# Performance work log

Measured on AMD Instinct MI355X. Metric: run time of the kernel, lower is better.

The kernel has to match this reference:

```python
import jax, jax.numpy as jnp
import numpy as np

EMB = 1024
HEAD = 64
B = 4
S = 4096


def setup_inputs() -> dict:
    key = jax.random.key(0)
    ks = jax.random.split(key, 7)
    std = 1.0 / np.sqrt(EMB)
    return {
        "x": jax.random.normal(ks[0], (B, S, EMB), dtype=jnp.float32),
        "Wq": jax.random.uniform(ks[1], (EMB, HEAD), jnp.float32, -std, std),
        "bq": jax.random.uniform(ks[2], (HEAD,), jnp.float32, -std, std),
        "Wk": jax.random.uniform(ks[3], (EMB, HEAD), jnp.float32, -std, std),
        "bk": jax.random.uniform(ks[4], (HEAD,), jnp.float32, -std, std),
        "Wv": jax.random.uniform(ks[5], (EMB, HEAD), jnp.float32, -std, std),
        "bv": jax.random.uniform(ks[6], (HEAD,), jnp.float32, -std, std),
    }


def reference(x, Wq, bq, Wk, bk, Wv, bv):
    # Q, K, V: [B, S, HEAD]
    Q = x @ Wq + bq
    K = x @ Wk + bk
    V = x @ Wv + bv
    scale = 1.0 / jnp.sqrt(jnp.asarray(HEAD, dtype=Q.dtype))
    # scores: [B, S, S]
    scores = jnp.einsum("bqd,bkd->bqk", Q, K) * scale
    seq = x.shape[1]
    # original mask = tril(randn) sliced; masked_fill where mask==0 => causal
    causal = jnp.tril(jnp.ones((seq, seq), dtype=bool))
    scores = jnp.where(causal, scores, -jnp.inf)
    attn = jax.nn.softmax(scores, axis=-1)
    return jnp.einsum("bqk,bkd->bqd", attn, V)
```

## Files before the change

### kernel.cpp

```cpp
#include <hip/hip_runtime.h>
#include <stdint.h>

#define S_LEN 4096
#define EMB   1024
#define HEAD  64

typedef short bf16x8 __attribute__((ext_vector_type(8)));
typedef float f32x4  __attribute__((ext_vector_type(4)));
typedef float f32x16 __attribute__((ext_vector_type(16)));

#define QSCALE 0.18033688011112042f

__device__ __forceinline__ unsigned short f2bf(float f) {
    union { float f; uint32_t u; } v; v.f = f;
    uint32_t r = v.u + 0x7fffu + ((v.u >> 16) & 1u);
    return (unsigned short)(r >> 16);
}

__device__ __forceinline__ int cvtpk_bf16(float lo, float hi_) {
    int r;
    asm("v_cvt_pk_bf16_f32 %0, %1, %2" : "=v"(r) : "v"(lo), "v"(hi_));
    return r;
}

__device__ __forceinline__ void gload_lds16(const void* g, void* l) {
    __builtin_amdgcn_global_load_lds(
        (const __attribute__((address_space(1))) void*)g,
        (__attribute__((address_space(3))) void*)l, 16, 0, 0);
}


__global__ void wprep_kernel(const float* __restrict__ Wq,
                             const float* __restrict__ Wk,
                             const float* __restrict__ Wv,
                             unsigned short* __restrict__ wt) {
    __shared__ float t[64][65];
    const int tid = threadIdx.x;
    const int m   = blockIdx.x >> 4;
    const int kcb = blockIdx.x & 15;
    const int k0  = kcb << 6;
    const float* W = (m == 0) ? Wq : (m == 1) ? Wk : Wv;
    for (int i = 0; i < 4; ++i) {
        const int k  = (tid >> 4) + i * 16;
        const int n4 = (tid & 15) << 2;
        float4 v = *(const float4*)&W[(k0 + k) * 64 + n4];
        t[k][n4 + 0] = v.x; t[k][n4 + 1] = v.y;
        t[k][n4 + 2] = v.z; t[k][n4 + 3] = v.w;
    }
    __syncthreads();
    const int n = tid >> 2, kq = (tid & 3) << 4;
    __align__(16) unsigned short u[16];
    for (int i = 0; i < 16; ++i) u[i] = f2bf(t[kq + i][n]);
    const int nimg = m * 64 + n;
    const int base = kcb * 12288 + nimg * 64;
    const int c0   = (kq >> 3) ^ (n & 7);
    const int c1   = ((kq >> 3) + 1) ^ (n & 7);
    *(int4*)&wt[base + c0 * 8] = *(int4*)&u[0];
    *(int4*)&wt[base + c1 * 8] = *(int4*)&u[8];
}

__global__ __launch_bounds__(512, 2) void qkv_kernel(
    const float* __restrict__ x, const unsigned short* __restrict__ wt,
    const float* __restrict__ bq, const float* __restrict__ bk,
    const float* __restrict__ bv,
    unsigned short* __restrict__ Qp, unsigned short* __restrict__ Kp,
    unsigned short* __restrict__ Vt) {

    __shared__ __align__(16) unsigned short xs[2][32 * 72];
    __shared__ __align__(16) unsigned short ws[2][12288];

    const int tid  = threadIdx.x;
    const int lane = tid & 63;
    const int w    = tid >> 6;
    const int wm   = w & 1;
    const int wn   = w >> 1;
    const int quad = lane >> 4;
    const int lid  = lane & 15;
    const int row0 = blockIdx.x * 32;

    f32x4 acc[3];
    for (int nf = 0; nf < 3; ++nf) acc[nf] = (f32x4){0.f, 0.f, 0.f, 0.f};

#define STAGE(BUF, KC)                                                         \
    do {                                                                       \
        {           \
            int rr = tid >> 4, c4 = (tid & 15) << 2;                           \
            float4 v = *(const float4*)&x[(row0 + rr) * EMB + (KC) * 64 + c4]; \
            ushort4 u;                                                         \
            u.x = f2bf(v.x); u.y = f2bf(v.y); u.z = f2bf(v.z); u.w = f2bf(v.w);\
            *(ushort4*)&xs[BUF][rr * 72 + c4] = u;                             \
        }                                                                      \
        {          \
            const unsigned short* gs = &wt[(KC) * 12288 + w * 1536 + lane * 8];\
            gload_lds16(gs,        &ws[BUF][w * 1536]);                        \
            gload_lds16(gs +  512, &ws[BUF][w * 1536 +  512]);                 \
            gload_lds16(gs + 1024, &ws[BUF][w * 1536 + 1024]);                 \
        }                                                                      \
    } while (0)

    STAGE(0, 0);
    __syncthreads();

    for (int kc = 0; kc < 16; ++kc) {
        const int cur = kc & 1;
        if (kc + 1 < 16) STAGE(cur ^ 1, kc + 1);
        for (int kk = 0; kk < 2; ++kk) {
            bf16x8 a = *(const bf16x8*)&xs[cur][(wm * 16 + lid) * 72 + kk * 32 + quad * 8];
            const int swz = ((((kk << 2) | quad) ^ (lid & 7)) << 3);
            for (int nf = 0; nf < 3; ++nf) {
                const int n = wn * 48 + nf * 16 + lid;
                bf16x8 bfr = *(const bf16x8*)&ws[cur][n * 64 + swz];
                acc[nf] = __builtin_amdgcn_mfma_f32_16x16x32_bf16(a, bfr, acc[nf], 0, 0, 0);
            }
        }
        __syncthreads();
    }
#undef STAGE

    for (int nf = 0; nf < 3; ++nf) {
        const int col = wn * 48 + nf * 16 + lid;
        const int mid = col >> 6;
        const int lc  = col & 63;
        const float bias = (mid == 0) ? bq[lc] : (mid == 1) ? bk[lc] : bv[lc];
        const int rb = row0 + wm * 16 + quad * 4;
        f32x4 v = acc[nf];
        if (mid < 2) {
            const int base = ((rb >> 5) << 11) + ((lc >> 3) << 8)
                           + ((rb & 31) << 3) + (lc & 7);
            unsigned short* P = (mid == 0) ? Qp : Kp;
            const float sc = (mid == 0) ? QSCALE : 1.0f;
            for (int j = 0; j < 4; ++j)
                P[base + j * 8] = f2bf((v[j] + bias) * sc);
        } else {
            const int bb = rb >> 12, s = rb & 4095;
            ushort4 u;
            u.x = f2bf(v[0] + bias); u.y = f2bf(v[1] + bias);
            u.z = f2bf(v[2] + bias); u.w = f2bf(v[3] + bias);
            *(ushort4*)&Vt[bb * 262144 + (s >> 3) * 512 + lc * 8 + (s & 7)] = u;
        }
    }
}

__global__ __launch_bounds__(512, 1) void flash_kernel(
    const unsigned short* __restrict__ Qp, const unsigned short* __restrict__ Kp,
    const unsigned short* __restrict__ Vt, float* __restrict__ out) {

    __shared__ __align__(16) float Obuf[8][32][66];
    __shared__ float lbuf[8][32];

    const int tid  = threadIdx.x;
    const int lane = tid & 63;
    const int w    = tid >> 6;
    const int hi   = lane >> 5;
    const int l5   = lane & 31;

    const int l  = blockIdx.x;
    const int x  = l & 7;
    const int b  = x & 3;
    const int p  = ((x >> 2) << 5) + (l >> 3);

    const unsigned short* Kb = &Kp[b * 262144];
    const unsigned short* Vb = &Vt[b * 262144];

    for (int half = 0; half < 2; ++half) {
        const int qt = half ? p : 127 - p;
        const int q0 = qt * 32;
        const int nt = qt + 1;

        bf16x8 qf[4];
#pragma unroll
        for (int dk = 0; dk < 4; ++dk)
            qf[dk] = *(const bf16x8*)&Qp[((b << 7) + qt) * 2048
                                         + (dk * 2 + hi) * 256 + l5 * 8];

        f32x16 O0 = {}, O1 = {};
        float ls = 0.f;

        int t = w;
        bf16x8 kf[4];
        if (t < nt) {
#pragma unroll
            for (int dk = 0; dk < 4; ++dk)
                kf[dk] = *(const bf16x8*)&Kb[t * 2048 + (dk * 2 + hi) * 256 + l5 * 8];
        }

        while (t < nt) {
            const int kt = t << 5;
            bf16x8 vf[2][2];
#pragma unroll
            for (int kc = 0; kc < 2; ++kc)
#pragma unroll
                for (int dh = 0; dh < 2; ++dh)
                    vf[dh][kc] = *(const bf16x8*)&Vb[(t * 4 + kc * 2 + hi) * 512
                                                     + (dh * 32 + l5) * 8];

            __builtin_amdgcn_s_setprio(1);
            f32x16 sa = {}, sb = {};
            sa = __builtin_amdgcn_mfma_f32_32x32x16_bf16(kf[0], qf[0], sa, 0, 0, 0);
            sb = __builtin_amdgcn_mfma_f32_32x32x16_bf16(kf[1], qf[1], sb, 0, 0, 0);
            sa = __builtin_amdgcn_mfma_f32_32x32x16_bf16(kf[2], qf[2], sa, 0, 0, 0);
            sb = __builtin_amdgcn_mfma_f32_32x32x16_bf16(kf[3], qf[3], sb, 0, 0, 0);
            __builtin_amdgcn_s_setprio(0);

            const int tn = t + 8;
            if (tn < nt) {
#pragma unroll
                for (int dk = 0; dk < 4; ++dk)
                    kf[dk] = *(const bf16x8*)&Kb[tn * 2048 + (dk * 2 + hi) * 256 + l5 * 8];
            }

            f32x16 st = sa + sb;

            if (t == nt - 1) {
#pragma unroll
                for (int rr = 0; rr < 16; ++rr) {
                    const int key = kt + (rr & 3) + 8 * (rr >> 2) + 4 * hi;
                    if (key > q0 + l5) st[rr] = -1e30f;
                }
            }

#pragma unroll
            for (int kc = 0; kc < 2; ++kc) {
                const int c8 = kc * 8;
                float ev[8];
#pragma unroll
                for (int i = 0; i < 8; ++i) ev[i] = __builtin_amdgcn_exp2f(st[c8 + i]);
                ls += ((ev[0] + ev[1]) + (ev[2] + ev[3])) +
                      ((ev[4] + ev[5]) + (ev[6] + ev[7]));
                const int p0 = cvtpk_bf16(ev[0], ev[1]);
                const int p1 = cvtpk_bf16(ev[2], ev[3]);
                const int p2 = cvtpk_bf16(ev[4], ev[5]);
                const int p3 = cvtpk_bf16(ev[6], ev[7]);
                auto s02 = __builtin_amdgcn_permlane32_swap(p0, p2, false, false);
                auto s13 = __builtin_amdgcn_permlane32_swap(p1, p3, false, false);
                union { int wd[4]; bf16x8 v; } pf;
                pf.wd[0] = s02[0]; pf.wd[1] = s13[0];
                pf.wd[2] = s02[1]; pf.wd[3] = s13[1];
                __builtin_amdgcn_s_setprio(1);
                O0 = __builtin_amdgcn_mfma_f32_32x32x16_bf16(pf.v, vf[0][kc], O0, 0, 0, 0);
                O1 = __builtin_amdgcn_mfma_f32_32x32x16_bf16(pf.v, vf[1][kc], O1, 0, 0, 0);
                __builtin_amdgcn_s_setprio(0);
            }
            t = tn;
        }

        const float lt = ls + __shfl_xor(ls, 32);
#pragma unroll
        for (int rr = 0; rr < 16; ++rr) {
            const int row = (rr & 3) + 8 * (rr >> 2) + 4 * hi;
            Obuf[w][row][l5]      = O0[rr];
            Obuf[w][row][32 + l5] = O1[rr];
        }
        if (lane < 32) lbuf[w][l5] = lt;
        __syncthreads();

        const int col = tid & 63;
        const int r0  = tid >> 6;
        for (int ii = 0; ii < 4; ++ii) {
            const int row = r0 + ii * 8;
            float o = 0.f, lsum = 0.f;
            for (int ww = 0; ww < 8; ++ww) {
                o    += Obuf[ww][row][col];
                lsum += lbuf[ww][row];
            }
            out[(b * S_LEN + q0 + row) * 64 + col] = o / lsum;
        }
        __syncthreads();
    }
}

extern "C" void kernel_launch(void* const* d_in, const int* in_sizes, int n_in,
                              void* d_out, int out_size, void* d_ws, size_t ws_size,
                              hipStream_t stream) {
    const float* x  = (const float*)d_in[0];
    const float* Wq = (const float*)d_in[1];
    const float* bq = (const float*)d_in[2];
    const float* Wk = (const float*)d_in[3];
    const float* bk = (const float*)d_in[4];
    const float* Wv = (const float*)d_in[5];
    const float* bv = (const float*)d_in[6];
    float* out = (float*)d_out;

    unsigned short* wt = (unsigned short*)d_ws;
    unsigned short* Qp = wt + 196608;
    unsigned short* Kp = Qp + 1048576;
    unsigned short* Vt = Kp + 1048576;

    hipLaunchKernelGGL(wprep_kernel, dim3(48), dim3(256), 0, stream, Wq, Wk, Wv, wt);
    hipLaunchKernelGGL(qkv_kernel, dim3(512), dim3(512), 0, stream,
                       x, wt, bq, bk, bv, Qp, Kp, Vt);
    hipLaunchKernelGGL(flash_kernel, dim3(256), dim3(512), 0, stream,
                       Qp, Kp, Vt, out);
}
```

Before: 132.4 us.

## Process paired high and low query tiles in one K/V pass

Restructures the flash kernel so each block handles its long (127-p) and short (p) query tiles together in a single sweep over key tiles. Each K and V fragment is then loaded once and reused for both query tiles instead of being reloaded in a second pass. The block-to-tile mapping also changes so adjacent blocks take neighbouring p values. In exchange, register pressure rises from holding two Q fragment sets and four output accumulators, which may cause spills at 512 threads.

```diff
diff --git a/kernel.cpp b/kernel.cpp
--- a/kernel.cpp
+++ b/kernel.cpp
@@ -141,6 +141,51 @@
     }
 }
 
+__device__ __forceinline__ void load_v(const unsigned short* Vb, int t,
+                                       int hi, int l5, bf16x8 (&vf)[2][2]) {
+#pragma unroll
+    for (int kc = 0; kc < 2; ++kc)
+#pragma unroll
+        for (int dh = 0; dh < 2; ++dh)
+            vf[dh][kc] = *(const bf16x8*)&Vb[(t * 4 + kc * 2 + hi) * 512
+                                             + (dh * 32 + l5) * 8];
+}
+
+__device__ __forceinline__ void mask_diag(f32x16& st, int kt, int q0,
+                                          int hi, int l5) {
+#pragma unroll
+    for (int rr = 0; rr < 16; ++rr) {
+        const int key = kt + (rr & 3) + 8 * (rr >> 2) + 4 * hi;
+        if (key > q0 + l5) st[rr] = -1e30f;
+    }
+}
+
+__device__ __forceinline__ void softmax_pv(const f32x16& st, const bf16x8 (&vf)[2][2],
+                                           f32x16& O0, f32x16& O1, float& ls) {
+#pragma unroll
+    for (int kc = 0; kc < 2; ++kc) {
+        const int c8 = kc * 8;
+        float ev[8];
+#pragma unroll
+        for (int i = 0; i < 8; ++i) ev[i] = __builtin_amdgcn_exp2f(st[c8 + i]);
+        ls += ((ev[0] + ev[1]) + (ev[2] + ev[3])) +
+              ((ev[4] + ev[5]) + (ev[6] + ev[7]));
+        const int p0 = cvtpk_bf16(ev[0], ev[1]);
+        const int p1 = cvtpk_bf16(ev[2], ev[3]);
+        const int p2 = cvtpk_bf16(ev[4], ev[5]);
+        const int p3 = cvtpk_bf16(ev[6], ev[7]);
+        auto s02 = __builtin_amdgcn_permlane32_swap(p0, p2, false, false);
+        auto s13 = __builtin_amdgcn_permlane32_swap(p1, p3, false, false);
+        union { int wd[4]; bf16x8 v; } pf;
+        pf.wd[0] = s02[0]; pf.wd[1] = s13[0];
+        pf.wd[2] = s02[1]; pf.wd[3] = s13[1];
+        __builtin_amdgcn_s_setprio(1);
+        O0 = __builtin_amdgcn_mfma_f32_32x32x16_bf16(pf.v, vf[0][kc], O0, 0, 0, 0);
+        O1 = __builtin_amdgcn_mfma_f32_32x32x16_bf16(pf.v, vf[1][kc], O1, 0, 0, 0);
+        __builtin_amdgcn_s_setprio(0);
+    }
+}
+
 __global__ __launch_bounds__(512, 1) void flash_kernel(
     const unsigned short* __restrict__ Qp, const unsigned short* __restrict__ Kp,
     const unsigned short* __restrict__ Vt, float* __restrict__ out) {
@@ -157,103 +202,84 @@
     const int l  = blockIdx.x;
     const int x  = l & 7;
     const int b  = x & 3;
-    const int p  = ((x >> 2) << 5) + (l >> 3);
+    const int p  = ((l >> 3) << 1) | (x >> 2);
+
+    const int qtH = 127 - p, qtL = p;
+    const int q0H = qtH << 5, q0L = qtL << 5;
+    const int ntH = qtH + 1;
+    const int ntL = qtL + 1;
 
     const unsigned short* Kb = &Kp[b * 262144];
     const unsigned short* Vb = &Vt[b * 262144];
 
-    for (int half = 0; half < 2; ++half) {
-        const int qt = half ? p : 127 - p;
-        const int q0 = qt * 32;
-        const int nt = qt + 1;
-
-        bf16x8 qf[4];
-#pragma unroll
-        for (int dk = 0; dk < 4; ++dk)
-            qf[dk] = *(const bf16x8*)&Qp[((b << 7) + qt) * 2048
-                                         + (dk * 2 + hi) * 256 + l5 * 8];
-
-        f32x16 O0 = {}, O1 = {};
-        float ls = 0.f;
-
-        int t = w;
-        bf16x8 kf[4];
-        if (t < nt) {
+    bf16x8 qfH[4], qfL[4];
+#pragma unroll
+    for (int dk = 0; dk < 4; ++dk) {
+        qfH[dk] = *(const bf16x8*)&Qp[((b << 7) + qtH) * 2048
+                                      + (dk * 2 + hi) * 256 + l5 * 8];
+        qfL[dk] = *(const bf16x8*)&Qp[((b << 7) + qtL) * 2048
+                                      + (dk * 2 + hi) * 256 + l5 * 8];
+    }
+
+    f32x16 OH0 = {}, OH1 = {}, OL0 = {}, OL1 = {};
+    float lsH = 0.f, lsL = 0.f;
+
+    int t = w;
+    bf16x8 kf[4];
+#pragma unroll
+    for (int dk = 0; dk < 4; ++dk)
+        kf[dk] = *(const bf16x8*)&Kb[t * 2048 + (dk * 2 + hi) * 256 + l5 * 8];
+
+    while (t < ntH) {
+        bf16x8 vf[2][2];
+        load_v(Vb, t, hi, l5, vf);
+
+        const bool doL = (t < ntL);
+
+        __builtin_amdgcn_s_setprio(1);
+        f32x16 sa = {}, sb = {};
+        sa = __builtin_amdgcn_mfma_f32_32x32x16_bf16(kf[0], qfH[0], sa, 0, 0, 0);
+        sb = __builtin_amdgcn_mfma_f32_32x32x16_bf16(kf[1], qfH[1], sb, 0, 0, 0);
+        sa = __builtin_amdgcn_mfma_f32_32x32x16_bf16(kf[2], qfH[2], sa, 0, 0, 0);
+        sb = __builtin_amdgcn_mfma_f32_32x32x16_bf16(kf[3], qfH[3], sb, 0, 0, 0);
+        f32x16 stH = sa + sb;
+        f32x16 stL = {};
+        if (doL) {
+            f32x16 la = {}, lb = {};
+            la = __builtin_amdgcn_mfma_f32_32x32x16_bf16(kf[0], qfL[0], la, 0, 0, 0);
+            lb = __builtin_amdgcn_mfma_f32_32x32x16_bf16(kf[1], qfL[1], lb, 0, 0, 0);
+            la = __builtin_amdgcn_mfma_f32_32x32x16_bf16(kf[2], qfL[2], la, 0, 0, 0);
+            lb = __builtin_amdgcn_mfma_f32_32x32x16_bf16(kf[3], qfL[3], lb, 0, 0, 0);
+            stL = la + lb;
+        }
+        __builtin_amdgcn_s_setprio(0);
+
+        const int tn = t + 8;
+        if (tn < ntH) {
 #pragma unroll
             for (int dk = 0; dk < 4; ++dk)
-                kf[dk] = *(const bf16x8*)&Kb[t * 2048 + (dk * 2 + hi) * 256 + l5 * 8];
-        }
-
-        while (t < nt) {
-            const int kt = t << 5;
-            bf16x8 vf[2][2];
-#pragma unroll
-            for (int kc = 0; kc < 2; ++kc)
-#pragma unroll
-                for (int dh = 0; dh < 2; ++dh)
-                    vf[dh][kc] = *(const bf16x8*)&Vb[(t * 4 + kc * 2 + hi) * 512
-                                                     + (dh * 32 + l5) * 8];
-
-            __builtin_amdgcn_s_setprio(1);
-            f32x16 sa = {}, sb = {};
-            sa = __builtin_amdgcn_mfma_f32_32x32x16_bf16(kf[0], qf[0], sa, 0, 0, 0);
-            sb = __builtin_amdgcn_mfma_f32_32x32x16_bf16(kf[1], qf[1], sb, 0, 0, 0);
-            sa = __builtin_amdgcn_mfma_f32_32x32x16_bf16(kf[2], qf[2], sa, 0, 0, 0);
-            sb = __builtin_amdgcn_mfma_f32_32x32x16_bf16(kf[3], qf[3], sb, 0, 0, 0);
-            __builtin_amdgcn_s_setprio(0);
-
-            const int tn = t + 8;
-            if (tn < nt) {
-#pragma unroll
-                for (int dk = 0; dk < 4; ++dk)
-                    kf[dk] = *(const bf16x8*)&Kb[tn * 2048 + (dk * 2 + hi) * 256 + l5 * 8];
-            }
-
-            f32x16 st = sa + sb;
-
-            if (t == nt - 1) {
-#pragma unroll
-                for (int rr = 0; rr < 16; ++rr) {
-                    const int key = kt + (rr & 3) + 8 * (rr >> 2) + 4 * hi;
-                    if (key > q0 + l5) st[rr] = -1e30f;
-                }
-            }
-
-#pragma unroll
-            for (int kc = 0; kc < 2; ++kc) {
-                const int c8 = kc * 8;
-                float ev[8];
-#pragma unroll
-                for (int i = 0; i < 8; ++i) ev[i] = __builtin_amdgcn_exp2f(st[c8 + i]);
-                ls += ((ev[0] + ev[1]) + (ev[2] + ev[3])) +
-                      ((ev[4] + ev[5]) + (ev[6] + ev[7]));
-                const int p0 = cvtpk_bf16(ev[0], ev[1]);
-                const int p1 = cvtpk_bf16(ev[2], ev[3]);
-                const int p2 = cvtpk_bf16(ev[4], ev[5]);
-                const int p3 = cvtpk_bf16(ev[6], ev[7]);
-                auto s02 = __builtin_amdgcn_permlane32_swap(p0, p2, false, false);
-                auto s13 = __builtin_amdgcn_permlane32_swap(p1, p3, false, false);
-                union { int wd[4]; bf16x8 v; } pf;
-                pf.wd[0] = s02[0]; pf.wd[1] = s13[0];
-                pf.wd[2] = s02[1]; pf.wd[3] = s13[1];
-                __builtin_amdgcn_s_setprio(1);
-                O0 = __builtin_amdgcn_mfma_f32_32x32x16_bf16(pf.v, vf[0][kc], O0, 0, 0, 0);
-                O1 = __builtin_amdgcn_mfma_f32_32x32x16_bf16(pf.v, vf[1][kc], O1, 0, 0, 0);
-                __builtin_amdgcn_s_setprio(0);
-            }
-            t = tn;
-        }
-
-        const float lt = ls + __shfl_xor(ls, 32);
+                kf[dk] = *(const bf16x8*)&Kb[tn * 2048 + (dk * 2 + hi) * 256 + l5 * 8];
+        }
+
+        if (t == ntH - 1) mask_diag(stH, t << 5, q0H, hi, l5);
+        softmax_pv(stH, vf, OH0, OH1, lsH);
+        if (doL) {
+            if (t == ntL - 1) mask_diag(stL, t << 5, q0L, hi, l5);
+            softmax_pv(stL, vf, OL0, OL1, lsL);
+        }
+        t = tn;
+    }
+
+    {
+        const float lt = lsH + __shfl_xor(lsH, 32);
 #pragma unroll
         for (int rr = 0; rr < 16; ++rr) {
             const int row = (rr & 3) + 8 * (rr >> 2) + 4 * hi;
-            Obuf[w][row][l5]      = O0[rr];
-            Obuf[w][row][32 + l5] = O1[rr];
+            Obuf[w][row][l5]      = OH0[rr];
+            Obuf[w][row][32 + l5] = OH1[rr];
         }
         if (lane < 32) lbuf[w][l5] = lt;
         __syncthreads();
-
         const int col = tid & 63;
         const int r0  = tid >> 6;
         for (int ii = 0; ii < 4; ++ii) {
@@ -263,9 +289,32 @@
                 o    += Obuf[ww][row][col];
                 lsum += lbuf[ww][row];
             }
-            out[(b * S_LEN + q0 + row) * 64 + col] = o / lsum;
+            out[(b * S_LEN + q0H + row) * 64 + col] = o / lsum;
         }
         __syncthreads();
+    }
+
+    {
+        const float lt = lsL + __shfl_xor(lsL, 32);
+#pragma unroll
+        for (int rr = 0; rr < 16; ++rr) {
+            const int row = (rr & 3) + 8 * (rr >> 2) + 4 * hi;
+            Obuf[w][row][l5]      = OL0[rr];
+            Obuf[w][row][32 + l5] = OL1[rr];
+        }
+        if (lane < 32) lbuf[w][l5] = lt;
+        __syncthreads();
+        const int col = tid & 63;
+        const int r0  = tid >> 6;
+        for (int ii = 0; ii < 4; ++ii) {
+            const int row = r0 + ii * 8;
+            float o = 0.f, lsum = 0.f;
+            for (int ww = 0; ww < 8; ++ww) {
+                o    += Obuf[ww][row][col];
+                lsum += lbuf[ww][row];
+            }
+            out[(b * S_LEN + q0L + row) * 64 + col] = o / lsum;
+        }
     }
 }
 
```

Result: no change. 133.4 us (+0.7%).
